# Kernel optimization log

Measured on AMD Instinct MI355X. Metric: run time of the kernel, lower is better.

The kernel has to match this reference:

```python
import jax, jax.numpy as jnp
import numpy as np

B, S, D = 4, 2048, 1024
H = 16
DK = D // H  # 64
F = 4096


def layer_norm(x, g, b, eps=1e-5):
    mu = jnp.mean(x, axis=-1, keepdims=True)
    var = jnp.mean(jnp.square(x - mu), axis=-1, keepdims=True)
    return (x - mu) * jax.lax.rsqrt(var + eps) * g + b


def setup_inputs() -> dict:
    key = jax.random.key(0)
    ks = jax.random.split(key, 12)
    s_in = 1.0 / np.sqrt(D)
    s_ff = 1.0 / np.sqrt(F)
    return {
        "x": jax.random.normal(ks[0], (B, S, D), jnp.float32),
        # per-head Q/K/V projections stacked: [H, D, DK]
        "Wq": jax.random.normal(ks[1], (H, D, DK), jnp.float32) * s_in,
        "bq": jnp.zeros((H, DK), jnp.float32),
        "Wk": jax.random.normal(ks[2], (H, D, DK), jnp.float32) * s_in,
        "bk": jnp.zeros((H, DK), jnp.float32),
        "Wv": jax.random.normal(ks[3], (H, D, DK), jnp.float32) * s_in,
        "bv": jnp.zeros((H, DK), jnp.float32),
        # output projection: [H*DK, D]
        "Wo": jax.random.normal(ks[4], (H * DK, D), jnp.float32) * s_in,
        "bo": jnp.zeros((D,), jnp.float32),
        "ln1_g": jnp.ones((D,), jnp.float32),
        "ln1_b": jnp.zeros((D,), jnp.float32),
        # FFN
        "W1": jax.random.normal(ks[5], (D, F), jnp.float32) * s_in,
        "b1": jnp.zeros((F,), jnp.float32),
        "W2": jax.random.normal(ks[6], (F, D), jnp.float32) * s_ff,
        "b2": jnp.zeros((D,), jnp.float32),
        "ln2_g": jnp.ones((D,), jnp.float32),
        "ln2_b": jnp.zeros((D,), jnp.float32),
    }


def reference(x, Wq, bq, Wk, bk, Wv, bv, Wo, bo, ln1_g, ln1_b,
              W1, b1, W2, b2, ln2_g, ln2_b):
    # --- multi-head attention (self-attention: q = k = v = x) ---
    q = jnp.einsum("bsd,hdk->bhsk", x, Wq) + bq[:, None, :]
    k = jnp.einsum("bsd,hdk->bhsk", x, Wk) + bk[:, None, :]
    v = jnp.einsum("bsd,hdk->bhsk", x, Wv) + bv[:, None, :]
    scale = 1.0 / jnp.sqrt(jnp.asarray(DK, x.dtype))
    scores = jnp.einsum("bhsk,bhtk->bhst", q, k) * scale  # [B,H,S,S]
    attn = jax.nn.softmax(scores, axis=-1)
    ctx = jnp.einsum("bhst,bhtk->bhsk", attn, v)           # [B,H,S,DK]
    # concat heads -> [B,S,H*DK], output projection
    ctx = jnp.transpose(ctx, (0, 2, 1, 3)).reshape(B, S, H * DK)
    attn_out = ctx @ Wo + bo
    # residual + post-LN (dropout is identity in eval mode)
    h = layer_norm(x + attn_out, ln1_g, ln1_b)
    # --- feed-forward (tanh activation) ---
    ff = jnp.tanh(h @ W1 + b1) @ W2 + b2
    return layer_norm(h + ff, ln2_g, ln2_b)
```

## Files before the change

### kernel.cpp

```cpp
#include <hip/hip_runtime.h>
#include <hip/hip_bf16.h>
#include <math.h>

typedef __attribute__((ext_vector_type(8))) short short8;
typedef __attribute__((ext_vector_type(4))) float f32x4;

#define NB 4
#define NS 2048
#define ND 1024
#define NH 16
#define NDK 64
#define NF 4096
#define NM (NB*NS)

#define QSCALE 0.18033688f

__device__ __forceinline__ unsigned short f2b(float f) {
  union { __hip_bfloat16 h; unsigned short u; } c;
  c.h = __float2bfloat16(f);
  return c.u;
}

__device__ __forceinline__ float b2f(unsigned short u) {
  union { float f; unsigned int i; } c;
  c.i = ((unsigned int)u) << 16;
  return c.f;
}

__device__ __forceinline__ void gload_lds16(const void* g, void* l) {
  __builtin_amdgcn_global_load_lds((const __attribute__((address_space(1))) void*)g,
                                   (__attribute__((address_space(3))) void*)l,
                                   16, 0, 0);
}

__device__ __forceinline__ float fast_tanh(float x) {
  float e = __builtin_amdgcn_exp2f(x * 2.885390082f);
  return 1.0f - 2.0f * __builtin_amdgcn_rcpf(e + 1.0f);
}

#define PREP_NBLK 20492

__global__ __launch_bounds__(256)
void prep_all(const float* __restrict__ x, unsigned short* __restrict__ x_bf,
              const float* __restrict__ Wq, const float* __restrict__ Wk,
              const float* __restrict__ Wv, unsigned short* __restrict__ Wqkvt,
              const float* __restrict__ Wo, unsigned short* __restrict__ Wot,
              const float* __restrict__ W1, unsigned short* __restrict__ W1t,
              const float* __restrict__ W2, unsigned short* __restrict__ W2t,
              const float* __restrict__ bq, const float* __restrict__ bk,
              const float* __restrict__ bv, float* __restrict__ bqkv)
{
  __shared__ float t[32][33];
  const int bid = blockIdx.x;
  const int tid = threadIdx.x;
  const int tx = tid & 31, ty = tid >> 5;

  if (bid < 8192) {
    int i = bid * 256 + tid;
    float4 v = ((const float4*)x)[i];
    ushort4 o;
    o.x = f2b(v.x); o.y = f2b(v.y); o.z = f2b(v.z); o.w = f2b(v.w);
    ((ushort4*)x_bf)[i] = o;
    return;
  }
  if (bid < 11264) {
    int idx = bid - 8192;
    int z = idx >> 6, y = (idx >> 5) & 1, xb = idx & 31;
    int which = z / 16, h = z % 16;
    const float* src = (which == 0 ? Wq : which == 1 ? Wk : Wv) + (size_t)h * ND * NDK;
    float scale = (which == 0) ? QSCALE : 1.0f;
    unsigned short* d = Wqkvt + (size_t)(which * 1024 + h * 64) * ND;
    int k0 = xb * 32, n0 = y * 32;
    for (int r = ty; r < 32; r += 8)
      t[r][tx] = src[(size_t)(k0 + r) * NDK + n0 + tx];
    __syncthreads();
    for (int r = ty; r < 32; r += 8)
      d[(size_t)(n0 + r) * ND + k0 + tx] = f2b(t[tx][r] * scale);
    return;
  }
  const float* src; unsigned short* dst; int ldsrc, lddst, k0, n0;
  if (bid < 12288) {
    int idx = bid - 11264; src = Wo; dst = Wot; ldsrc = 1024; lddst = 1024;
    k0 = (idx & 31) * 32; n0 = (idx >> 5) * 32;
  } else if (bid < 16384) {
    int idx = bid - 12288; src = W1; dst = W1t; ldsrc = 4096; lddst = 1024;
    k0 = (idx & 31) * 32; n0 = (idx >> 5) * 32;
  } else if (bid < 20480) {
    int idx = bid - 16384; src = W2; dst = W2t; ldsrc = 1024; lddst = 4096;
    k0 = (idx >> 5) * 32; n0 = (idx & 31) * 32;
  } else {
    int i = (bid - 20480) * 256 + tid;
    if (i < 3072) {
      float v = (i < 1024) ? bq[i] * QSCALE : (i < 2048 ? bk[i - 1024] : bv[i - 2048]);
      bqkv[i] = v;
    }
    return;
  }
  for (int r = ty; r < 32; r += 8)
    t[r][tx] = src[(size_t)(k0 + r) * ldsrc + n0 + tx];
  __syncthreads();
  for (int r = ty; r < 32; r += 8)
    dst[(size_t)(n0 + r) * lddst + k0 + tx] = f2b(t[tx][r]);
}

__global__ __launch_bounds__(256)
void transpose_v(const unsigned short* __restrict__ qkv, unsigned short* __restrict__ vt) {
  __shared__ unsigned short t[32][33];
  int bh = blockIdx.z; int b = bh >> 4, h = bh & 15;
  int s0 = blockIdx.x * 32;
  int d0 = blockIdx.y * 32;
  int tx = threadIdx.x, ty = threadIdx.y;
  for (int r = ty; r < 32; r += 8)
    t[r][tx] = qkv[(size_t)(b * NS + s0 + r) * 3072 + 2048 + h * 64 + d0 + tx];
  __syncthreads();
  for (int r = ty; r < 32; r += 8)
    vt[((size_t)bh * 64 + d0 + r) * NS + s0 + tx] = t[tx][r];
}


template<int EPI>
__global__ __launch_bounds__(512, 1)
void gemm_bt(const unsigned short* __restrict__ A, const unsigned short* __restrict__ Bt,
             const float* __restrict__ bias, void* __restrict__ Cout,
             int M, int N, int K)
{
  __shared__ __align__(16) unsigned short As[2][256 * 64];
  __shared__ __align__(16) unsigned short Bs[2][128 * 64];

  const int nwg = gridDim.x;
  const int id = blockIdx.x;
  const int swz = (id & 7) * (nwg >> 3) + (id >> 3);
  const int nbx = N >> 7;
  const int mb = swz / nbx, nb = swz % nbx;
  const int m0 = mb * 256;
  const int n0 = nb * 128;

  const int tid = threadIdx.x;
  const int wave = tid >> 6, lane = tid & 63;
  const int l16 = lane & 15, lhi = lane >> 4;
  const int wr = wave >> 1, wc = wave & 1;

  const int rowL = lane >> 3;
  const int gg = (lane & 7) ^ rowL;

  f32x4 acc[4][4] = {};

  auto STAGE = [&](int buf, int kt) {
    const int k0 = kt * 64;
#pragma unroll
    for (int c = wave * 4; c < wave * 4 + 4; ++c)
      gload_lds16(A + (size_t)(m0 + c * 8 + rowL) * K + (k0 + gg * 8), &As[buf][c * 512]);
#pragma unroll
    for (int c = wave * 2; c < wave * 2 + 2; ++c)
      gload_lds16(Bt + (size_t)(n0 + c * 8 + rowL) * K + (k0 + gg * 8), &Bs[buf][c * 512]);
  };

  auto COMPUTE = [&](int buf) {
    const char* as = (const char*)&As[buf][0];
    const char* bs = (const char*)&Bs[buf][0];
    short8 af[4][2], bf[4][2];
#pragma unroll
    for (int i = 0; i < 4; ++i) {
      const int row = wr * 64 + i * 16 + l16;
      const char* rb = as + row * 128;
#pragma unroll
      for (int ks = 0; ks < 2; ++ks)
        af[i][ks] = *(const short8*)(rb + (((ks * 4 + lhi) ^ (row & 7)) << 4));
    }
#pragma unroll
    for (int j = 0; j < 4; ++j) {
      const int row = wc * 64 + j * 16 + l16;
      const char* rb = bs + row * 128;
#pragma unroll
      for (int ks = 0; ks < 2; ++ks)
        bf[j][ks] = *(const short8*)(rb + (((ks * 4 + lhi) ^ (row & 7)) << 4));
    }
    __builtin_amdgcn_s_setprio(1);
#pragma unroll
    for (int i = 0; i < 4; ++i)
#pragma unroll
      for (int j = 0; j < 4; ++j)
#pragma unroll
        for (int ks = 0; ks < 2; ++ks)
          acc[i][j] = __builtin_amdgcn_mfma_f32_16x16x32_bf16(af[i][ks], bf[j][ks],
                                                              acc[i][j], 0, 0, 0);
    __builtin_amdgcn_s_setprio(0);
  };

  const int NT = K >> 6;
  STAGE(0, 0);
  __syncthreads();
  for (int j = 0; j < NT; j += 2) {
    STAGE(1, j + 1);
    COMPUTE(0);
    __syncthreads();
    if (j + 2 < NT) STAGE(0, j + 2);
    COMPUTE(1);
    __syncthreads();
  }

#pragma unroll
  for (int i = 0; i < 4; ++i) {
    const int row = m0 + wr * 64 + i * 16 + lhi * 4;
#pragma unroll
    for (int j = 0; j < 4; ++j) {
      const int col = n0 + wc * 64 + j * 16 + l16;
      const float bv = bias[col];
#pragma unroll
      for (int r = 0; r < 4; ++r) {
        float v = acc[i][j][r] + bv;
        size_t idx = (size_t)(row + r) * N + col;
        if (EPI == 0)      ((unsigned short*)Cout)[idx] = f2b(v);
        else if (EPI == 1) ((float*)Cout)[idx] = v;
        else               ((unsigned short*)Cout)[idx] = f2b(fast_tanh(v));
      }
    }
  }
}


template<int EPI>
__global__ __launch_bounds__(512, 2)
void gemm256(const unsigned short* __restrict__ A, const unsigned short* __restrict__ Bt,
             const float* __restrict__ bias, void* __restrict__ Cout,
             int M, int N, int K)
{
  __shared__ __align__(16) unsigned short As[2][256 * 32];
  __shared__ __align__(16) unsigned short Bs[2][256 * 32];

  const int nwg = gridDim.x;
  const int id = blockIdx.x;
  const int swz = (id & 7) * (nwg >> 3) + (id >> 3);
  const int nbx = N >> 8;
  const int mb = swz / nbx, nb = swz % nbx;
  const int m0 = mb * 256;
  const int n0 = nb * 256;

  const int tid = threadIdx.x;
  const int wave = tid >> 6, lane = tid & 63;
  const int l16 = lane & 15, lhi = lane >> 4;
  const int wr = wave >> 2, wc = wave & 3;

  const int rowL = lane >> 2;
  const int sg = (lane & 3) ^ (rowL & 3);

  f32x4 acc[8][4] = {};

  auto STAGE = [&](int buf, int kt) {
    const int k0 = kt * 32;
#pragma unroll
    for (int c = wave * 2; c < wave * 2 + 2; ++c) {
      gload_lds16(A + (size_t)(m0 + c * 16 + rowL) * K + (k0 + sg * 8), &As[buf][c * 512]);
      gload_lds16(Bt + (size_t)(n0 + c * 16 + rowL) * K + (k0 + sg * 8), &Bs[buf][c * 512]);
    }
  };

  auto COMPUTE = [&](int buf) {
    const char* as = (const char*)&As[buf][0];
    const char* bs = (const char*)&Bs[buf][0];
    short8 bf[4];
#pragma unroll
    for (int j = 0; j < 4; ++j) {
      const int row = wc * 64 + j * 16 + l16;
      bf[j] = *(const short8*)(bs + row * 64 + ((lhi ^ (row & 3)) << 4));
    }
#pragma unroll
    for (int i = 0; i < 8; ++i) {
      const int row = wr * 128 + i * 16 + l16;
      short8 af = *(const short8*)(as + row * 64 + ((lhi ^ (row & 3)) << 4));
      __builtin_amdgcn_s_setprio(1);
#pragma unroll
      for (int j = 0; j < 4; ++j)
        acc[i][j] = __builtin_amdgcn_mfma_f32_16x16x32_bf16(af, bf[j], acc[i][j], 0, 0, 0);
      __builtin_amdgcn_s_setprio(0);
    }
  };

  const int NT = K >> 5;
  STAGE(0, 0);
  __syncthreads();
  for (int j = 0; j < NT; j += 2) {
    STAGE(1, j + 1);
    COMPUTE(0);
    __syncthreads();
    if (j + 2 < NT) STAGE(0, j + 2);
    COMPUTE(1);
    __syncthreads();
  }

#pragma unroll
  for (int i = 0; i < 8; ++i) {
    const int row = m0 + wr * 128 + i * 16 + lhi * 4;
#pragma unroll
    for (int j = 0; j < 4; ++j) {
      const int col = n0 + wc * 64 + j * 16 + l16;
      const float bv = bias[col];
#pragma unroll
      for (int r = 0; r < 4; ++r) {
        float v = acc[i][j][r] + bv;
        size_t idx = (size_t)(row + r) * N + col;
        if (EPI == 0)      ((unsigned short*)Cout)[idx] = f2b(v);
        else if (EPI == 1) ((float*)Cout)[idx] = v;
        else               ((unsigned short*)Cout)[idx] = f2b(fast_tanh(v));
      }
    }
  }
}


__global__ __launch_bounds__(512)
void attn_fwd(const unsigned short* __restrict__ qkv, const unsigned short* __restrict__ vtg,
              unsigned short* __restrict__ ctx)
{
  const int id = blockIdx.x;
  const int swz = (id & 7) * 64 + (id >> 3);
  const int qt = swz & 7;
  const int bh = swz >> 3;
  const int b = bh >> 4, h = bh & 15;
  const int row0 = b * NS + qt * 256;
  const int tid = threadIdx.x;
  const int wave = tid >> 6, lane = tid & 63;
  const int l16 = lane & 15, lhi = lane >> 4;

  __shared__ __align__(16) unsigned short Ks[2][64 * 64];
  __shared__ __align__(16) unsigned short Vs[2][64 * 64];
  __shared__ __align__(16) unsigned short Ps[16][16 * 64];

  const unsigned short* kbase = qkv + ND + (size_t)h * 64;
  const unsigned short* vbase = vtg + (size_t)bh * 64 * NS;

  const int r0 = tid >> 3;
  const int f0 = ((tid & 7) ^ (r0 & 7)) * 8;
  const int ldsb0 = wave * 512;

  const int lbase = l16 * 128;
  const int xs = (l16 & 7) << 4;
  const int kvo0 = (lhi * 16) ^ xs;
  const int kvo1 = (64 + lhi * 16) ^ xs;
  int pjo[4];
#pragma unroll
  for (int j = 0; j < 4; ++j)
    pjo[j] = (j * 32 + lhi * 8) ^ xs;

  short8 ones8;
#pragma unroll
  for (int e = 0; e < 8; ++e) ones8[e] = (short)0x3F80;

  short8 qf[2][2];
#pragma unroll
  for (int sub = 0; sub < 2; ++sub) {
    const unsigned short* qrow =
        qkv + (size_t)(row0 + wave * 32 + sub * 16 + l16) * 3072 + h * 64;
    qf[sub][0] = *(const short8*)(qrow + lhi * 8);
    qf[sub][1] = *(const short8*)(qrow + 32 + lhi * 8);
  }

  f32x4 o[2][4] = {};
  f32x4 o5[2] = {};

  auto STAGE = [&](int buf, int kt) {
    const size_t kr = (size_t)(b * NS + kt * 64);
    const int kb64 = kt * 64;
    gload_lds16(kbase + (kr + r0) * 3072 + f0, &Ks[buf][ldsb0]);
    gload_lds16(vbase + (size_t)r0 * NS + kb64 + f0, &Vs[buf][ldsb0]);
  };

  auto COMPUTE = [&](int buf) {
    const char* kb = (const char*)&Ks[buf][0];
    const char* vb = (const char*)&Vs[buf][0];
    char* pb0 = (char*)&Ps[wave * 2 + 0][0];
    char* pb1 = (char*)&Ps[wave * 2 + 1][0];

    f32x4 s[2][4] = {};
    __builtin_amdgcn_s_setprio(1);
#pragma unroll
    for (int c = 0; c < 2; ++c) {
      const int kvo = c ? kvo1 : kvo0;
#pragma unroll
      for (int j = 0; j < 4; ++j) {
        short8 kf = *(const short8*)(kb + lbase + j * 2048 + kvo);
        s[0][j] = __builtin_amdgcn_mfma_f32_16x16x32_bf16(kf, qf[0][c], s[0][j], 0, 0, 0);
        s[1][j] = __builtin_amdgcn_mfma_f32_16x16x32_bf16(kf, qf[1][c], s[1][j], 0, 0, 0);
      }
    }
    __builtin_amdgcn_s_setprio(0);

#pragma unroll
    for (int sub = 0; sub < 2; ++sub) {
      char* pb = sub ? pb1 : pb0;
#pragma unroll
      for (int j = 0; j < 4; ++j) {
#pragma unroll
        for (int r = 0; r < 4; ++r)
          s[sub][j][r] = __builtin_amdgcn_exp2f(s[sub][j][r]);
        unsigned int lo = (unsigned int)f2b(s[sub][j][0]) | ((unsigned int)f2b(s[sub][j][1]) << 16);
        unsigned int hi = (unsigned int)f2b(s[sub][j][2]) | ((unsigned int)f2b(s[sub][j][3]) << 16);
        unsigned long long w = (unsigned long long)lo | ((unsigned long long)hi << 32);
        *(unsigned long long*)(pb + lbase + pjo[j]) = w;
      }
    }

    __builtin_amdgcn_s_setprio(1);
#pragma unroll
    for (int c = 0; c < 2; ++c) {
      const int kvo = c ? kvo1 : kvo0;
      short8 pf0 = *(const short8*)(pb0 + lbase + kvo);
      short8 pf1 = *(const short8*)(pb1 + lbase + kvo);
#pragma unroll
      for (int j = 0; j < 4; ++j) {
        short8 vf = *(const short8*)(vb + lbase + j * 2048 + kvo);
        o[0][j] = __builtin_amdgcn_mfma_f32_16x16x32_bf16(pf0, vf, o[0][j], 0, 0, 0);
        o[1][j] = __builtin_amdgcn_mfma_f32_16x16x32_bf16(pf1, vf, o[1][j], 0, 0, 0);
      }
      o5[0] = __builtin_amdgcn_mfma_f32_16x16x32_bf16(pf0, ones8, o5[0], 0, 0, 0);
      o5[1] = __builtin_amdgcn_mfma_f32_16x16x32_bf16(pf1, ones8, o5[1], 0, 0, 0);
    }
    __builtin_amdgcn_s_setprio(0);
  };

  STAGE(0, 0);
  __syncthreads();
  for (int kt = 0; kt < NS / 64; kt += 2) {
    STAGE(1, kt + 1);
    COMPUTE(0);
    __syncthreads();
    if (kt + 2 < NS / 64) STAGE(0, kt + 2);
    COMPUTE(1);
    __syncthreads();
  }

#pragma unroll
  for (int sub = 0; sub < 2; ++sub) {
    float rinv[4];
#pragma unroll
    for (int r = 0; r < 4; ++r) rinv[r] = 1.0f / o5[sub][r];
#pragma unroll
    for (int j = 0; j < 4; ++j)
#pragma unroll
      for (int r = 0; r < 4; ++r) {
        const int row = row0 + wave * 32 + sub * 16 + lhi * 4 + r;
        ctx[(size_t)row * ND + h * 64 + j * 16 + l16] = f2b(o[sub][j][r] * rinv[r]);
      }
  }
}


template<int OUTF32>
__global__ __launch_bounds__(256)
void ln_fused(const unsigned short* __restrict__ xa, const unsigned short* __restrict__ xb,
              const float* __restrict__ g, const float* __restrict__ beta, void* out_)
{
  const int row = blockIdx.x;
  const int tid = threadIdx.x;
  const int wave = tid >> 6, lane = tid & 63;
  __shared__ float r1[4], r2[4];

  ushort4 au = ((const ushort4*)(xa + (size_t)row * ND))[tid];
  ushort4 bu = ((const ushort4*)(xb + (size_t)row * ND))[tid];
  float v0 = b2f(au.x) + b2f(bu.x), v1 = b2f(au.y) + b2f(bu.y);
  float v2 = b2f(au.z) + b2f(bu.z), v3 = b2f(au.w) + b2f(bu.w);

  float sm = v0 + v1 + v2 + v3;
#pragma unroll
  for (int d = 1; d < 64; d <<= 1) sm += __shfl_xor(sm, d);
  if (lane == 0) r1[wave] = sm;
  __syncthreads();
  const float mu = (r1[0] + r1[1] + r1[2] + r1[3]) * (1.0f / ND);
  const float d0 = v0 - mu, d1 = v1 - mu, d2 = v2 - mu, d3 = v3 - mu;
  float vs = d0 * d0 + d1 * d1 + d2 * d2 + d3 * d3;
#pragma unroll
  for (int d = 1; d < 64; d <<= 1) vs += __shfl_xor(vs, d);
  if (lane == 0) r2[wave] = vs;
  __syncthreads();
  const float var = (r2[0] + r2[1] + r2[2] + r2[3]) * (1.0f / ND);
  const float inv = rsqrtf(var + 1e-5f);
  float4 gg = ((const float4*)g)[tid];
  float4 bb = ((const float4*)beta)[tid];
  float o0 = d0 * inv * gg.x + bb.x;
  float o1 = d1 * inv * gg.y + bb.y;
  float o2 = d2 * inv * gg.z + bb.z;
  float o3 = d3 * inv * gg.w + bb.w;
  if (OUTF32 == 0) {
    ushort4 w; w.x = f2b(o0); w.y = f2b(o1); w.z = f2b(o2); w.w = f2b(o3);
    ((ushort4*)((unsigned short*)out_ + (size_t)row * ND))[tid] = w;
  } else {
    float4 ov; ov.x = o0; ov.y = o1; ov.z = o2; ov.w = o3;
    ((float4*)((float*)out_ + (size_t)row * ND))[tid] = ov;
  }
}


extern "C" void kernel_launch(void* const* d_in, const int* in_sizes, int n_in,
                              void* d_out, int out_size, void* d_ws, size_t ws_size,
                              hipStream_t stream)
{
  (void)in_sizes; (void)n_in; (void)out_size; (void)ws_size;
  const float* x   = (const float*)d_in[0];
  const float* Wq  = (const float*)d_in[1];
  const float* bq  = (const float*)d_in[2];
  const float* Wk  = (const float*)d_in[3];
  const float* bk  = (const float*)d_in[4];
  const float* Wv  = (const float*)d_in[5];
  const float* bv  = (const float*)d_in[6];
  const float* Wo  = (const float*)d_in[7];
  const float* bo  = (const float*)d_in[8];
  const float* g1  = (const float*)d_in[9];
  const float* be1 = (const float*)d_in[10];
  const float* W1  = (const float*)d_in[11];
  const float* b1  = (const float*)d_in[12];
  const float* W2  = (const float*)d_in[13];
  const float* b2  = (const float*)d_in[14];
  const float* g2  = (const float*)d_in[15];
  const float* be2 = (const float*)d_in[16];

  char* ws = (char*)d_ws;
  const size_t MB = 1ull << 20;
  unsigned short* x_bf  = (unsigned short*)(ws);
  unsigned short* qkv   = (unsigned short*)(ws + 16 * MB);
  unsigned short* aout  = (unsigned short*)(ws + 16 * MB);
  unsigned short* ff1   = (unsigned short*)(ws);
  unsigned short* ctx   = (unsigned short*)(ws + 64 * MB);
  unsigned short* h_bf  = (unsigned short*)(ws + 64 * MB);
  unsigned short* Wqkvt = (unsigned short*)(ws + 80 * MB);
  unsigned short* Wot   = (unsigned short*)(ws + 86 * MB);
  unsigned short* W1t   = (unsigned short*)(ws + 88 * MB);
  unsigned short* W2t   = (unsigned short*)(ws + 96 * MB);
  float*          bqkv  = (float*)(ws + 104 * MB);
  unsigned short* ffout = (unsigned short*)(ws + 105 * MB);
  unsigned short* vtg   = (unsigned short*)(ws + 121 * MB);

  prep_all<<<PREP_NBLK, 256, 0, stream>>>(x, x_bf, Wq, Wk, Wv, Wqkvt,
                                          Wo, Wot, W1, W1t, W2, W2t,
                                          bq, bk, bv, bqkv);

  gemm_bt<0><<<(NM / 256) * (3072 / 128), 512, 0, stream>>>(x_bf, Wqkvt, bqkv, qkv, NM, 3072, 1024);
  transpose_v<<<dim3(64, 2, 64), dim3(32, 8), 0, stream>>>(qkv, vtg);
  attn_fwd<<<512, 512, 0, stream>>>(qkv, vtg, ctx);
  gemm_bt<0><<<(NM / 256) * (1024 / 128), 512, 0, stream>>>(ctx, Wot, bo, aout, NM, 1024, 1024);
  ln_fused<0><<<NM, 256, 0, stream>>>(x_bf, aout, g1, be1, h_bf);
  gemm256<2><<<(NM / 256) * (4096 / 256), 512, 0, stream>>>(h_bf, W1t, b1, ff1, NM, 4096, 1024);
  gemm_bt<0><<<(NM / 256) * (1024 / 128), 512, 0, stream>>>(ff1, W2t, b2, ffout, NM, 1024, 4096);
  ln_fused<1><<<NM, 256, 0, stream>>>(h_bf, ffout, g2, be2, (float*)d_out);
}
```

Measured before the change: 419.6 us.

## Triple-buffer gemm_bt LDS pipeline and route FFN1 through gemm_bt

Replaces the double-buffered K loop in gemm_bt with a three-stage LDS ring. Two tiles are kept in flight, and explicit vmcnt waits plus raw s_barrier replace __syncthreads, so each barrier waits only for the oldest load. This aims to hide more global-load latency behind MFMA work. The separate gemm256 kernel is removed and the FFN1 GEMM now uses gemm_bt with 256x128 tiles. LDS use grows to about 144KB per block, and the raw barrier and waitcnt sequencing risks hazards if the compiler reorders other memory operations.

```diff
diff --git a/kernel.cpp b/kernel.cpp
--- a/kernel.cpp
+++ b/kernel.cpp
@@ -124,8 +124,8 @@
              const float* __restrict__ bias, void* __restrict__ Cout,
              int M, int N, int K)
 {
-  __shared__ __align__(16) unsigned short As[2][256 * 64];
-  __shared__ __align__(16) unsigned short Bs[2][128 * 64];
+  __shared__ __align__(16) unsigned short As[3][256 * 64];
+  __shared__ __align__(16) unsigned short Bs[3][128 * 64];
 
   const int nwg = gridDim.x;
   const int id = blockIdx.x;
@@ -145,19 +145,17 @@
 
   f32x4 acc[4][4] = {};
 
-  auto STAGE = [&](int buf, int kt) {
+  auto STAGE = [&](unsigned short* la, unsigned short* lb, int kt) {
     const int k0 = kt * 64;
 #pragma unroll
     for (int c = wave * 4; c < wave * 4 + 4; ++c)
-      gload_lds16(A + (size_t)(m0 + c * 8 + rowL) * K + (k0 + gg * 8), &As[buf][c * 512]);
+      gload_lds16(A + (size_t)(m0 + c * 8 + rowL) * K + (k0 + gg * 8), la + c * 512);
 #pragma unroll
     for (int c = wave * 2; c < wave * 2 + 2; ++c)
-      gload_lds16(Bt + (size_t)(n0 + c * 8 + rowL) * K + (k0 + gg * 8), &Bs[buf][c * 512]);
+      gload_lds16(Bt + (size_t)(n0 + c * 8 + rowL) * K + (k0 + gg * 8), lb + c * 512);
   };
 
-  auto COMPUTE = [&](int buf) {
-    const char* as = (const char*)&As[buf][0];
-    const char* bs = (const char*)&Bs[buf][0];
+  auto COMPUTE = [&](const char* as, const char* bs) {
     short8 af[4][2], bf[4][2];
 #pragma unroll
     for (int i = 0; i < 4; ++i) {
@@ -187,110 +185,30 @@
     __builtin_amdgcn_s_setprio(0);
   };
 
+  unsigned short *a0 = &As[0][0], *a1 = &As[1][0], *a2 = &As[2][0];
+  unsigned short *b0 = &Bs[0][0], *b1 = &Bs[1][0], *b2 = &Bs[2][0];
+
   const int NT = K >> 6;
-  STAGE(0, 0);
-  __syncthreads();
-  for (int j = 0; j < NT; j += 2) {
-    STAGE(1, j + 1);
-    COMPUTE(0);
-    __syncthreads();
-    if (j + 2 < NT) STAGE(0, j + 2);
-    COMPUTE(1);
-    __syncthreads();
+  STAGE(a0, b0, 0);
+  STAGE(a1, b1, 1);
+  asm volatile("s_waitcnt vmcnt(6)" ::: "memory");
+  asm volatile("s_barrier" ::: "memory");
+
+  for (int t = 0; t < NT; ++t) {
+    if (t + 2 < NT) STAGE(a2, b2, t + 2);
+    COMPUTE((const char*)a0, (const char*)b0);
+    if (t + 1 < NT) {
+      if (t + 2 < NT) { asm volatile("s_waitcnt vmcnt(6)" ::: "memory"); }
+      else            { asm volatile("s_waitcnt vmcnt(0)" ::: "memory"); }
+      asm volatile("s_barrier" ::: "memory");
+    }
+    unsigned short* ta = a0; a0 = a1; a1 = a2; a2 = ta;
+    unsigned short* tb = b0; b0 = b1; b1 = b2; b2 = tb;
   }
 
 #pragma unroll
   for (int i = 0; i < 4; ++i) {
     const int row = m0 + wr * 64 + i * 16 + lhi * 4;
-#pragma unroll
-    for (int j = 0; j < 4; ++j) {
-      const int col = n0 + wc * 64 + j * 16 + l16;
-      const float bv = bias[col];
-#pragma unroll
-      for (int r = 0; r < 4; ++r) {
-        float v = acc[i][j][r] + bv;
-        size_t idx = (size_t)(row + r) * N + col;
-        if (EPI == 0)      ((unsigned short*)Cout)[idx] = f2b(v);
-        else if (EPI == 1) ((float*)Cout)[idx] = v;
-        else               ((unsigned short*)Cout)[idx] = f2b(fast_tanh(v));
-      }
-    }
-  }
-}
-
-
-template<int EPI>
-__global__ __launch_bounds__(512, 2)
-void gemm256(const unsigned short* __restrict__ A, const unsigned short* __restrict__ Bt,
-             const float* __restrict__ bias, void* __restrict__ Cout,
-             int M, int N, int K)
-{
-  __shared__ __align__(16) unsigned short As[2][256 * 32];
-  __shared__ __align__(16) unsigned short Bs[2][256 * 32];
-
-  const int nwg = gridDim.x;
-  const int id = blockIdx.x;
-  const int swz = (id & 7) * (nwg >> 3) + (id >> 3);
-  const int nbx = N >> 8;
-  const int mb = swz / nbx, nb = swz % nbx;
-  const int m0 = mb * 256;
-  const int n0 = nb * 256;
-
-  const int tid = threadIdx.x;
-  const int wave = tid >> 6, lane = tid & 63;
-  const int l16 = lane & 15, lhi = lane >> 4;
-  const int wr = wave >> 2, wc = wave & 3;
-
-  const int rowL = lane >> 2;
-  const int sg = (lane & 3) ^ (rowL & 3);
-
-  f32x4 acc[8][4] = {};
-
-  auto STAGE = [&](int buf, int kt) {
-    const int k0 = kt * 32;
-#pragma unroll
-    for (int c = wave * 2; c < wave * 2 + 2; ++c) {
-      gload_lds16(A + (size_t)(m0 + c * 16 + rowL) * K + (k0 + sg * 8), &As[buf][c * 512]);
-      gload_lds16(Bt + (size_t)(n0 + c * 16 + rowL) * K + (k0 + sg * 8), &Bs[buf][c * 512]);
-    }
-  };
-
-  auto COMPUTE = [&](int buf) {
-    const char* as = (const char*)&As[buf][0];
-    const char* bs = (const char*)&Bs[buf][0];
-    short8 bf[4];
-#pragma unroll
-    for (int j = 0; j < 4; ++j) {
-      const int row = wc * 64 + j * 16 + l16;
-      bf[j] = *(const short8*)(bs + row * 64 + ((lhi ^ (row & 3)) << 4));
-    }
-#pragma unroll
-    for (int i = 0; i < 8; ++i) {
-      const int row = wr * 128 + i * 16 + l16;
-      short8 af = *(const short8*)(as + row * 64 + ((lhi ^ (row & 3)) << 4));
-      __builtin_amdgcn_s_setprio(1);
-#pragma unroll
-      for (int j = 0; j < 4; ++j)
-        acc[i][j] = __builtin_amdgcn_mfma_f32_16x16x32_bf16(af, bf[j], acc[i][j], 0, 0, 0);
-      __builtin_amdgcn_s_setprio(0);
-    }
-  };
-
-  const int NT = K >> 5;
-  STAGE(0, 0);
-  __syncthreads();
-  for (int j = 0; j < NT; j += 2) {
-    STAGE(1, j + 1);
-    COMPUTE(0);
-    __syncthreads();
-    if (j + 2 < NT) STAGE(0, j + 2);
-    COMPUTE(1);
-    __syncthreads();
-  }
-
-#pragma unroll
-  for (int i = 0; i < 8; ++i) {
-    const int row = m0 + wr * 128 + i * 16 + lhi * 4;
 #pragma unroll
     for (int j = 0; j < 4; ++j) {
       const int col = n0 + wc * 64 + j * 16 + l16;
@@ -538,7 +456,7 @@
   attn_fwd<<<512, 512, 0, stream>>>(qkv, vtg, ctx);
   gemm_bt<0><<<(NM / 256) * (1024 / 128), 512, 0, stream>>>(ctx, Wot, bo, aout, NM, 1024, 1024);
   ln_fused<0><<<NM, 256, 0, stream>>>(x_bf, aout, g1, be1, h_bf);
-  gemm256<2><<<(NM / 256) * (4096 / 256), 512, 0, stream>>>(h_bf, W1t, b1, ff1, NM, 4096, 1024);
+  gemm_bt<2><<<(NM / 256) * (4096 / 128), 512, 0, stream>>>(h_bf, W1t, b1, ff1, NM, 4096, 1024);
   gemm_bt<0><<<(NM / 256) * (1024 / 128), 512, 0, stream>>>(ff1, W2t, b2, ffout, NM, 1024, 4096);
   ln_fused<1><<<NM, 256, 0, stream>>>(h_bf, ffout, g2, be2, (float*)d_out);
 }
```

Result: slower. 431.8 us (+2.9%).
